# Kernel optimization log

Hardware: AMD Instinct MI355X
Metric: run time of the kernel (lower is better)

## Reference

```python
import jax, jax.numpy as jnp
import numpy as np

B, S, DM, DC = 16, 4096, 1280, 768
N_AOE, N_IMG, N_DELTA = 16, 16, 16
ANAT_GATE, DIS_GATE, DELTA_SCALE = 0.5, 0.5, 1.0


def setup_inputs() -> dict:
    key = jax.random.key(0)
    ks = jax.random.split(key, 9)
    def lin(k, fan_in, fan_out):
        return jax.random.normal(k, (fan_in, fan_out), jnp.float32) / np.sqrt(fan_in)
    return {
        "hidden_states": jax.random.normal(ks[0], (B, S, DM), jnp.float32),
        "encoder_hidden_states": jax.random.normal(ks[1], (B, N_AOE + N_IMG + N_DELTA, DC), jnp.float32),
        "w_q": lin(ks[2], DM, DM),
        "w_k": lin(ks[3], DC, DM),
        "w_v": lin(ks[4], DC, DM),
        "w_k_dis": lin(ks[5], DC, DM),
        "w_v_dis": lin(ks[6], DC, DM),
        "w_out": lin(ks[7], DM, DM),
        "b_out": jnp.zeros((DM,), jnp.float32),
        "n_heads": 8,
    }


def _heads(x, h):
    b, s, d = x.shape
    return x.reshape(b, s, h, d // h).transpose(0, 2, 1, 3)  # [B,H,S,dh]


def _attend(q, k, v, scale):
    # q:[B,H,Sq,dh], k/v:[B,H,Sk,dh], Sk small (16)
    scores = jnp.einsum("bhqd,bhkd->bhqk", q, k) * scale
    probs = jax.nn.softmax(scores, axis=-1)
    return jnp.einsum("bhqk,bhkd->bhqd", probs, v)


def reference(hidden_states, encoder_hidden_states, w_q, w_k, w_v,
              w_k_dis, w_v_dis, w_out, b_out, n_heads):
    residual = hidden_states
    dh = DM // n_heads
    scale = 1.0 / np.sqrt(dh)

    dis_tok = encoder_hidden_states[:, :N_AOE, :]
    anat_tok = encoder_hidden_states[:, N_AOE:N_AOE + N_IMG, :]
    delta_tok = encoder_hidden_states[:, -N_DELTA:, :]

    q = _heads(hidden_states @ w_q, n_heads)
    z_anat = _attend(q, _heads(anat_tok @ w_k, n_heads), _heads(anat_tok @ w_v, n_heads), scale)
    z_dis = _attend(q, _heads(dis_tok @ w_k_dis, n_heads), _heads(dis_tok @ w_v_dis, n_heads), scale)
    z_delta = _attend(q, _heads(delta_tok @ w_k_dis, n_heads), _heads(delta_tok @ w_v_dis, n_heads), scale)

    z = ANAT_GATE * z_anat + DIS_GATE * z_dis + DELTA_SCALE * z_delta
    out = z.transpose(0, 2, 1, 3).reshape(hidden_states.shape[0], -1, DM)
    out = out @ w_out + b_out  # to_out[0]; to_out[1] dropout = identity in eval
    return out + residual  # residual_connection, rescale_output_factor=1.0
```

## Files before the change

kernel.cpp:

```cpp
#include <hip/hip_runtime.h>
#include <hip/hip_bf16.h>

#define B_ 16
#define S_ 4096
#define DM_ 1280
#define DC_ 768
#define NC_ 384
#define SCALE_ 0.07905694150420949f

typedef __attribute__((ext_vector_type(8))) short bf16x8;
typedef __attribute__((ext_vector_type(4))) float f32x4;
typedef __attribute__((ext_vector_type(4))) unsigned short u16x4;

#define S_BARRIER() asm volatile("s_barrier" ::: "memory")
#define WAIT_VM(n) asm volatile("s_waitcnt vmcnt(" #n ")" ::: "memory")
#define WAIT_LGKM0() asm volatile("s_waitcnt lgkmcnt(0)" ::: "memory")

__device__ __forceinline__ unsigned short f2bf(float f) {
    unsigned int u = __builtin_bit_cast(unsigned int, f);
    u = (u + 0x7FFFu + ((u >> 16) & 1u)) >> 16;
    return (unsigned short)u;
}

__device__ __forceinline__ bf16x8 pack8(float4 x0, float4 x1) {
    bf16x8 a;
    a[0] = __builtin_bit_cast(short, __float2bfloat16(x0.x));
    a[1] = __builtin_bit_cast(short, __float2bfloat16(x0.y));
    a[2] = __builtin_bit_cast(short, __float2bfloat16(x0.z));
    a[3] = __builtin_bit_cast(short, __float2bfloat16(x0.w));
    a[4] = __builtin_bit_cast(short, __float2bfloat16(x1.x));
    a[5] = __builtin_bit_cast(short, __float2bfloat16(x1.y));
    a[6] = __builtin_bit_cast(short, __float2bfloat16(x1.z));
    a[7] = __builtin_bit_cast(short, __float2bfloat16(x1.w));
    return a;
}

__device__ __forceinline__ void gload16(const void* g, void* l) {
    __builtin_amdgcn_global_load_lds(
        (const __attribute__((address_space(1))) void*)g,
        (__attribute__((address_space(3))) void*)l, 16, 0, 0);
}

__device__ __forceinline__ void tcvt_body(const float* __restrict__ in,
                                          unsigned short* __restrict__ out,
                                          int R, int C, int bx, int by, int tid) {
    __shared__ float tile[32][33];
    int c0 = bx * 32, r0 = by * 32;
    int tx = tid & 31, ty = tid >> 5;
    for (int i = ty; i < 32; i += 8)
        tile[i][tx] = in[(size_t)(r0 + i) * C + c0 + tx];
    __syncthreads();
    for (int i = ty; i < 32; i += 8)
        out[(size_t)(c0 + i) * R + r0 + tx] = f2bf(tile[tx][i]);
}

__global__ __launch_bounds__(256)
void k_prep(const float* __restrict__ wq, const float* __restrict__ wk,
            const float* __restrict__ wv, const float* __restrict__ wkd,
            const float* __restrict__ wvd, const float* __restrict__ wout,
            unsigned short* __restrict__ wq_bf, unsigned short* __restrict__ wTk,
            unsigned short* __restrict__ wTv, unsigned short* __restrict__ wTkd,
            unsigned short* __restrict__ wTvd, unsigned short* __restrict__ woutT) {
    int bid = blockIdx.x, tid = threadIdx.x;
    if (bid < 1600) {
        int i = bid * 256 + tid;
        float4 v = ((const float4*)wq)[i];
        u16x4 o = { f2bf(v.x), f2bf(v.y), f2bf(v.z), f2bf(v.w) };
        ((u16x4*)wq_bf)[i] = o;
    } else if (bid < 2560) {
        int r = bid - 1600; tcvt_body(wk,  wTk,  DC_, DM_, r % 40, r / 40, tid);
    } else if (bid < 3520) {
        int r = bid - 2560; tcvt_body(wv,  wTv,  DC_, DM_, r % 40, r / 40, tid);
    } else if (bid < 4480) {
        int r = bid - 3520; tcvt_body(wkd, wTkd, DC_, DM_, r % 40, r / 40, tid);
    } else if (bid < 5440) {
        int r = bid - 4480; tcvt_body(wvd, wTvd, DC_, DM_, r % 40, r / 40, tid);
    } else {
        int r = bid - 5440; tcvt_body(wout, woutT, DM_, DM_, r % 40, r / 40, tid);
    }
}

__global__ __launch_bounds__(256)
void k_projM(const float* __restrict__ enc,
             const unsigned short* __restrict__ wTk, const unsigned short* __restrict__ wTv,
             const unsigned short* __restrict__ wTkd, const unsigned short* __restrict__ wTvd,
             unsigned short* __restrict__ KV) {
    int bid = blockIdx.x;
    int j = bid / 80, rem = bid % 80, b = rem / 5, nt = rem % 5;
    int tid = threadIdx.x, w = tid >> 6, l = tid & 63, l15 = l & 15, l4 = l >> 4;
    int tok0 = (j < 2) ? 16 : ((j < 4) ? 0 : 32);
    const unsigned short* wT = (j == 0) ? wTk : (j == 1) ? wTv : (j == 2 || j == 4) ? wTkd : wTvd;
    const float* ap = enc + ((size_t)(b * 48 + tok0 + l15)) * DC_;
    f32x4 zero = {0.f, 0.f, 0.f, 0.f};
    f32x4 acc[4];
    #pragma unroll
    for (int t = 0; t < 4; t++) acc[t] = zero;
    for (int kk = 0; kk < 24; kk++) {
        const float4* hp = (const float4*)(ap + kk * 32 + l4 * 8);
        bf16x8 af = pack8(hp[0], hp[1]);
        #pragma unroll
        for (int t = 0; t < 4; t++) {
            int n0 = nt * 256 + w * 64 + t * 16;
            bf16x8 bf = *(const bf16x8*)(wT + (size_t)(n0 + l15) * DC_ + kk * 32 + l4 * 8);
            acc[t] = __builtin_amdgcn_mfma_f32_16x16x32_bf16(af, bf, acc[t], 0, 0, 0);
        }
    }
    #pragma unroll
    for (int t = 0; t < 4; t++) {
        int e = nt * 256 + w * 64 + t * 16 + l15;
        #pragma unroll
        for (int r = 0; r < 4; r++)
            KV[((size_t)(j * 16 + b) * 16 + l4 * 4 + r) * DM_ + e] = f2bf(acc[t][r]);
    }
}

__global__ __launch_bounds__(256)
void k_au(const unsigned short* __restrict__ KV, const unsigned short* __restrict__ wqbf,
          const unsigned short* __restrict__ woutT,
          unsigned short* __restrict__ At2, unsigned short* __restrict__ Ut2) {
    int bid0 = blockIdx.x;
    bool isA = bid0 < 384;
    int bid = isA ? bid0 : bid0 - 384;
    int b = bid & 15, r_ = bid >> 4, x = r_ >> 3, h = r_ & 7;
    int tid = threadIdx.x, w = tid >> 6, l = tid & 63, l15 = l & 15, l4 = l >> 4;
    int xh = x * 8 + h;
    int jrow = isA ? (2 * x) : (2 * x + 1);
    const unsigned short* wmat = isA ? wqbf : woutT;
    float postscale = isA ? SCALE_ : ((x == 2) ? 1.0f : 0.5f);
    bf16x8 bfr[5];
    #pragma unroll
    for (int kk = 0; kk < 5; kk++)
        bfr[kk] = *(const bf16x8*)(KV + ((size_t)(jrow * 16 + b) * 16 + l15) * DM_ + h * 160 + kk * 32 + l4 * 8);
    f32x4 zero = {0.f, 0.f, 0.f, 0.f};
    for (int tt = 0; tt < 20; tt++) {
        int d0 = w * 320 + tt * 16;
        f32x4 acc = zero;
        if (isA) {
            #pragma unroll
            for (int kk = 0; kk < 5; kk++) {
                bf16x8 af = *(const bf16x8*)(wmat + (size_t)(d0 + l15) * DM_ + h * 160 + kk * 32 + l4 * 8);
                acc = __builtin_amdgcn_mfma_f32_16x16x32_bf16(af, bfr[kk], acc, 0, 0, 0);
            }
            int c = xh * 16 + l15;
            u16x4 pk;
            #pragma unroll
            for (int r = 0; r < 4; r++) pk[r] = f2bf(acc[r] * postscale);
            *(u16x4*)(At2 + ((size_t)(b * 40 + (d0 >> 5)) * NC_ + c) * 32 + (d0 & 31) + l4 * 4) = pk;
        } else {
            #pragma unroll
            for (int kk = 0; kk < 5; kk++) {
                bf16x8 af = *(const bf16x8*)(wmat + (size_t)(d0 + l15) * DM_ + h * 160 + kk * 32 + l4 * 8);
                acc = __builtin_amdgcn_mfma_f32_16x16x32_bf16(bfr[kk], af, acc, 0, 0, 0);
            }
            int e = d0 + l15;
            u16x4 pk;
            #pragma unroll
            for (int r = 0; r < 4; r++) pk[r] = f2bf(acc[r] * postscale);
            *(u16x4*)(Ut2 + ((size_t)(b * 12 + (xh >> 1)) * DM_ + e) * 32 + (xh & 1) * 16 + l4 * 4) = pk;
        }
    }
}

__global__ __launch_bounds__(256, 2)
void k_scores7(const float* __restrict__ hid, const unsigned short* __restrict__ At2,
               unsigned short* __restrict__ P2) {
    __shared__ char smem[73728];
    unsigned short* Apnl = (unsigned short*)smem;
    char* Hlds = smem + 49152;
    int bid = blockIdx.x;
    int orig = (bid & 7) * 128 + (bid >> 3);
    int b = orig >> 6, st = orig & 63;
    int s0 = st * 64;
    int tid = threadIdx.x, w = tid >> 6, l = tid & 63, l15 = l & 15, l4 = l >> 4;
    int rdsw = (l4 ^ ((l15 >> 1) & 3)) * 8;
    const unsigned short* Ab = At2 + (size_t)b * 40 * NC_ * 32;
    const float* hsrc = hid + ((size_t)b * S_ + s0) * DM_;
    f32x4 zero = {0.f, 0.f, 0.f, 0.f};
    f32x4 acc[4][6];
    #pragma unroll
    for (int si = 0; si < 4; si++)
        #pragma unroll
        for (int cj = 0; cj < 6; cj++) acc[si][cj] = zero;

    auto stageA = [&](int kk, int ab) {
        const unsigned short* slab = Ab + (size_t)kk * (NC_ * 32);
        #pragma unroll
        for (int i = 0; i < 6; i++) {
            int idx = i * 256 + tid;
            int c = idx >> 2, m = (idx & 3) ^ ((c >> 1) & 3);
            gload16(slab + (size_t)c * 32 + m * 8, smem + ab * 24576 + idx * 16);
        }
    };
    auto stageH = [&](int kk, int hb) {
        #pragma unroll
        for (int i = 0; i < 2; i++) {
            int idx = i * 256 + tid;
            int r = idx >> 3, sg = (idx & 7) ^ (r & 7);
            gload16(hsrc + (size_t)r * DM_ + kk * 32 + sg * 4, Hlds + hb * 8192 + idx * 16);
        }
    };
    auto compute = [&](int ab, int hb) {
        bf16x8 hpk[4];
        #pragma unroll
        for (int si = 0; si < 4; si++) {
            int r = si * 16 + l15;
            float4 lo = *(const float4*)(Hlds + hb * 8192 + r * 128 + (((2 * l4) ^ (l15 & 7)) * 16));
            float4 hi = *(const float4*)(Hlds + hb * 8192 + r * 128 + (((2 * l4 + 1) ^ (l15 & 7)) * 16));
            hpk[si] = pack8(lo, hi);
        }
        __builtin_amdgcn_s_setprio(1);
        #pragma unroll
        for (int cj = 0; cj < 6; cj++) {
            bf16x8 af = *(const bf16x8*)&Apnl[ab * 12288 + (w * 96 + cj * 16 + l15) * 32 + rdsw];
            #pragma unroll
            for (int si = 0; si < 4; si++)
                acc[si][cj] = __builtin_amdgcn_mfma_f32_16x16x32_bf16(af, hpk[si], acc[si][cj], 0, 0, 0);
        }
        __builtin_amdgcn_s_setprio(0);
    };
    auto SITER = [&](int kk) {
        stageA(kk + 1, (kk + 1) & 1);
        stageH(kk + 2, (kk + 2) % 3);
        WAIT_VM(10);
        S_BARRIER();
        compute(kk & 1, kk % 3);
        WAIT_LGKM0();
        S_BARRIER();
    };

    stageA(0, 0); stageH(0, 0); stageH(1, 1);
    for (int k0 = 0; k0 < 36; k0 += 6) {
        SITER(k0 + 0); SITER(k0 + 1); SITER(k0 + 2);
        SITER(k0 + 3); SITER(k0 + 4); SITER(k0 + 5);
    }
    SITER(36); SITER(37);
    stageA(39, 1);
    WAIT_VM(8);
    S_BARRIER();
    compute(0, 38 % 3);
    WAIT_LGKM0();
    S_BARRIER();
    WAIT_VM(0);
    S_BARRIER();
    compute(1, 39 % 3);
    WAIT_LGKM0();
    S_BARRIER();

    #pragma unroll
    for (int si = 0; si < 4; si++) {
        int s_l = si * 16 + l15;
        #pragma unroll
        for (int cj = 0; cj < 6; cj++) {
            float v0 = acc[si][cj][0], v1 = acc[si][cj][1], v2 = acc[si][cj][2], v3 = acc[si][cj][3];
            float mx = fmaxf(fmaxf(v0, v1), fmaxf(v2, v3));
            mx = fmaxf(mx, __shfl_xor(mx, 16));
            mx = fmaxf(mx, __shfl_xor(mx, 32));
            float e0 = __expf(v0 - mx), e1 = __expf(v1 - mx), e2 = __expf(v2 - mx), e3 = __expf(v3 - mx);
            float sm = e0 + e1 + e2 + e3;
            sm += __shfl_xor(sm, 16);
            sm += __shfl_xor(sm, 32);
            float rs = 1.0f / sm;
            u16x4 pk = { f2bf(e0 * rs), f2bf(e1 * rs), f2bf(e2 * rs), f2bf(e3 * rs) };
            int c = w * 96 + cj * 16 + l4 * 4;
            int chunk = ((c & 31) >> 3) ^ (s_l & 3);
            *(u16x4*)(smem + (c >> 5) * 4096 + s_l * 64 + chunk * 16 + (l4 & 1) * 8) = pk;
        }
    }
    __syncthreads();

    unsigned short* P2b = P2 + (size_t)b * 12 * S_ * 32;
    #pragma unroll
    for (int i = 0; i < 12; i++) {
        int sl = tid >> 2, m = tid & 3;
        uint4 v = *(const uint4*)(smem + i * 4096 + sl * 64 + ((m ^ (sl & 3)) * 16));
        *(uint4*)(P2b + ((size_t)i * S_ + s0 + sl) * 32 + m * 8) = v;
    }
}

__global__ __launch_bounds__(256, 3)
void k_pv4(const unsigned short* __restrict__ P2, const unsigned short* __restrict__ Ut2,
           const float* __restrict__ hid, const float* __restrict__ bo,
           float* __restrict__ out) {
    __shared__ unsigned short Plds[3 * 4096];
    __shared__ unsigned short Ulds[3 * 4096];
    int bid = blockIdx.x;
    int orig = (bid & 7) * 640 + (bid >> 3);
    int b = orig / 320, rem = orig % 320;
    int st = rem / 10, ec = rem % 10;
    int s0 = st * 128, e0 = ec * 128;
    int tid = threadIdx.x, w = tid >> 6, l = tid & 63, l15 = l & 15, l4 = l >> 4;
    int wr = w >> 1, wc = w & 1;
    int rdsw = (l4 ^ ((l15 >> 1) & 3)) * 8;
    const unsigned short* Pb = P2 + (size_t)b * 12 * S_ * 32;
    const unsigned short* Ub = Ut2 + (size_t)b * 12 * DM_ * 32;
    f32x4 zero = {0.f, 0.f, 0.f, 0.f};
    f32x4 acc[4][4];
    #pragma unroll
    for (int si = 0; si < 4; si++)
        #pragma unroll
        for (int ej = 0; ej < 4; ej++) acc[si][ej] = zero;

    auto stage = [&](int kk, int bufsel) {
        const unsigned short* Pslab = Pb + (size_t)kk * S_ * 32;
        const unsigned short* Uslab = Ub + (size_t)kk * DM_ * 32;
        #pragma unroll
        for (int i = 0; i < 2; i++) {
            int idx = i * 256 + tid;
            int r = idx >> 2, m = (idx & 3) ^ ((r >> 1) & 3);
            gload16(Pslab + ((size_t)s0 + r) * 32 + m * 8, (char*)Plds + bufsel * 8192 + idx * 16);
            gload16(Uslab + ((size_t)e0 + r) * 32 + m * 8, (char*)Ulds + bufsel * 8192 + idx * 16);
        }
    };
    auto compute = [&](int cur) {
        bf16x8 uf[4], pf[4];
        #pragma unroll
        for (int ej = 0; ej < 4; ej++)
            uf[ej] = *(const bf16x8*)&Ulds[cur * 4096 + (wr * 64 + ej * 16 + l15) * 32 + rdsw];
        #pragma unroll
        for (int si = 0; si < 4; si++)
            pf[si] = *(const bf16x8*)&Plds[cur * 4096 + (wc * 64 + si * 16 + l15) * 32 + rdsw];
        __builtin_amdgcn_s_setprio(1);
        #pragma unroll
        for (int si = 0; si < 4; si++)
            #pragma unroll
            for (int ej = 0; ej < 4; ej++)
                acc[si][ej] = __builtin_amdgcn_mfma_f32_16x16x32_bf16(uf[ej], pf[si], acc[si][ej], 0, 0, 0);
        __builtin_amdgcn_s_setprio(0);
    };
    auto PITER = [&](int kk, int cur, int tgt) {
        stage(kk + 2, tgt);
        WAIT_VM(8);
        S_BARRIER();
        compute(cur);
        WAIT_LGKM0();
        S_BARRIER();
    };

    stage(0, 0); stage(1, 1);
    for (int k0 = 0; k0 < 9; k0 += 3) {
        PITER(k0 + 0, 0, 2); PITER(k0 + 1, 1, 0); PITER(k0 + 2, 2, 1);
    }
    PITER(9, 0, 2);
    WAIT_VM(4); S_BARRIER(); compute(1); WAIT_LGKM0(); S_BARRIER();
    WAIT_VM(0); S_BARRIER(); compute(2);

    float4 b4[4];
    #pragma unroll
    for (int ej = 0; ej < 4; ej++)
        b4[ej] = *(const float4*)(bo + e0 + wr * 64 + ej * 16 + l4 * 4);
    #pragma unroll
    for (int si = 0; si < 4; si++) {
        int srow = s0 + wc * 64 + si * 16 + l15;
        #pragma unroll
        for (int ej = 0; ej < 4; ej++) {
            int ecol = e0 + wr * 64 + ej * 16 + l4 * 4;
            size_t off = ((size_t)b * S_ + srow) * DM_ + ecol;
            float4 h4 = *(const float4*)(hid + off);
            f32x4 a = acc[si][ej];
            float4 o4;
            o4.x = a[0] + b4[ej].x + h4.x;
            o4.y = a[1] + b4[ej].y + h4.y;
            o4.z = a[2] + b4[ej].z + h4.z;
            o4.w = a[3] + b4[ej].w + h4.w;
            *(float4*)(out + off) = o4;
        }
    }
}

extern "C" void kernel_launch(void* const* d_in, const int* in_sizes, int n_in,
                              void* d_out, int out_size, void* d_ws, size_t ws_size,
                              hipStream_t stream) {
    const float* hid  = (const float*)d_in[0];
    const float* enc  = (const float*)d_in[1];
    const float* wq   = (const float*)d_in[2];
    const float* wk   = (const float*)d_in[3];
    const float* wv   = (const float*)d_in[4];
    const float* wkd  = (const float*)d_in[5];
    const float* wvd  = (const float*)d_in[6];
    const float* wout = (const float*)d_in[7];
    const float* bo   = (const float*)d_in[8];
    float* out = (float*)d_out;

    char* ws = (char*)d_ws;
    unsigned short* At2    = (unsigned short*)(ws);
    unsigned short* Ut2    = (unsigned short*)(ws + 15728640);
    unsigned short* KV     = (unsigned short*)(ws + 31457280);
    unsigned short* wq_bf  = (unsigned short*)(ws + 35389440);
    unsigned short* woutT  = (unsigned short*)(ws + 38666240);
    unsigned short* wTk    = (unsigned short*)(ws + 41943040);
    unsigned short* wTv    = (unsigned short*)(ws + 43909120);
    unsigned short* wTkd   = (unsigned short*)(ws + 45875200);
    unsigned short* wTvd   = (unsigned short*)(ws + 47841280);
    unsigned short* P2     = (unsigned short*)(ws + 35389440);

    k_prep<<<7040, 256, 0, stream>>>(wq, wk, wv, wkd, wvd, wout,
                                     wq_bf, wTk, wTv, wTkd, wTvd, woutT);
    k_projM<<<480, 256, 0, stream>>>(enc, wTk, wTv, wTkd, wTvd, KV);
    k_au<<<768, 256, 0, stream>>>(KV, wq_bf, woutT, At2, Ut2);
    k_scores7<<<1024, 256, 0, stream>>>(hid, At2, P2);
    k_pv4<<<5120, 256, 0, stream>>>(P2, Ut2, hid, bo, out);
}
```

Before: 399.6 us.

## Double sequence tile in scores kernel to reuse A panel across 128 rows

The scores kernel now processes 128 sequence rows per block instead of 64, so each staged A panel slab feeds twice as many MFMAs and global A traffic is halved. The hidden-state pipeline drops from triple to double buffering, and the softmax output is written directly to global memory instead of being staged through LDS. The costs are doubled accumulator registers (48 f32x4) at two blocks per CU, half as many blocks, a shallower prefetch depth, and narrower 8-byte global stores for P.

```diff
diff --git a/kernel.cpp b/kernel.cpp
--- a/kernel.cpp
+++ b/kernel.cpp
@@ -162,25 +162,25 @@
 }
 
 __global__ __launch_bounds__(256, 2)
-void k_scores7(const float* __restrict__ hid, const unsigned short* __restrict__ At2,
+void k_scores8(const float* __restrict__ hid, const unsigned short* __restrict__ At2,
                unsigned short* __restrict__ P2) {
-    __shared__ char smem[73728];
+    __shared__ char smem[81920];
     unsigned short* Apnl = (unsigned short*)smem;
     char* Hlds = smem + 49152;
     int bid = blockIdx.x;
-    int orig = (bid & 7) * 128 + (bid >> 3);
-    int b = orig >> 6, st = orig & 63;
-    int s0 = st * 64;
+    int orig = (bid & 7) * 64 + (bid >> 3);
+    int b = orig >> 5, st = orig & 31;
+    int s0 = st * 128;
     int tid = threadIdx.x, w = tid >> 6, l = tid & 63, l15 = l & 15, l4 = l >> 4;
     int rdsw = (l4 ^ ((l15 >> 1) & 3)) * 8;
     const unsigned short* Ab = At2 + (size_t)b * 40 * NC_ * 32;
     const float* hsrc = hid + ((size_t)b * S_ + s0) * DM_;
     f32x4 zero = {0.f, 0.f, 0.f, 0.f};
-    f32x4 acc[4][6];
-    #pragma unroll
-    for (int si = 0; si < 4; si++)
-        #pragma unroll
-        for (int cj = 0; cj < 6; cj++) acc[si][cj] = zero;
+    f32x4 acc[8][6];
+    #pragma unroll
+    for (int g = 0; g < 8; g++)
+        #pragma unroll
+        for (int cj = 0; cj < 6; cj++) acc[g][cj] = zero;
 
     auto stageA = [&](int kk, int ab) {
         const unsigned short* slab = Ab + (size_t)kk * (NC_ * 32);
@@ -193,65 +193,58 @@
     };
     auto stageH = [&](int kk, int hb) {
         #pragma unroll
-        for (int i = 0; i < 2; i++) {
+        for (int i = 0; i < 4; i++) {
             int idx = i * 256 + tid;
             int r = idx >> 3, sg = (idx & 7) ^ (r & 7);
-            gload16(hsrc + (size_t)r * DM_ + kk * 32 + sg * 4, Hlds + hb * 8192 + idx * 16);
+            gload16(hsrc + (size_t)r * DM_ + kk * 32 + sg * 4, Hlds + hb * 16384 + idx * 16);
         }
     };
     auto compute = [&](int ab, int hb) {
-        bf16x8 hpk[4];
-        #pragma unroll
-        for (int si = 0; si < 4; si++) {
-            int r = si * 16 + l15;
-            float4 lo = *(const float4*)(Hlds + hb * 8192 + r * 128 + (((2 * l4) ^ (l15 & 7)) * 16));
-            float4 hi = *(const float4*)(Hlds + hb * 8192 + r * 128 + (((2 * l4 + 1) ^ (l15 & 7)) * 16));
-            hpk[si] = pack8(lo, hi);
-        }
-        __builtin_amdgcn_s_setprio(1);
-        #pragma unroll
-        for (int cj = 0; cj < 6; cj++) {
-            bf16x8 af = *(const bf16x8*)&Apnl[ab * 12288 + (w * 96 + cj * 16 + l15) * 32 + rdsw];
-            #pragma unroll
-            for (int si = 0; si < 4; si++)
-                acc[si][cj] = __builtin_amdgcn_mfma_f32_16x16x32_bf16(af, hpk[si], acc[si][cj], 0, 0, 0);
-        }
-        __builtin_amdgcn_s_setprio(0);
+        #pragma unroll
+        for (int sh = 0; sh < 2; sh++) {
+            bf16x8 hpk[4];
+            #pragma unroll
+            for (int si = 0; si < 4; si++) {
+                int r = sh * 64 + si * 16 + l15;
+                float4 lo = *(const float4*)(Hlds + hb * 16384 + r * 128 + (((2 * l4) ^ (l15 & 7)) * 16));
+                float4 hi = *(const float4*)(Hlds + hb * 16384 + r * 128 + (((2 * l4 + 1) ^ (l15 & 7)) * 16));
+                hpk[si] = pack8(lo, hi);
+            }
+            __builtin_amdgcn_s_setprio(1);
+            #pragma unroll
+            for (int cj = 0; cj < 6; cj++) {
+                bf16x8 af = *(const bf16x8*)&Apnl[ab * 12288 + (w * 96 + cj * 16 + l15) * 32 + rdsw];
+                #pragma unroll
+                for (int si = 0; si < 4; si++)
+                    acc[sh * 4 + si][cj] = __builtin_amdgcn_mfma_f32_16x16x32_bf16(af, hpk[si], acc[sh * 4 + si][cj], 0, 0, 0);
+            }
+            __builtin_amdgcn_s_setprio(0);
+        }
     };
     auto SITER = [&](int kk) {
         stageA(kk + 1, (kk + 1) & 1);
-        stageH(kk + 2, (kk + 2) % 3);
+        stageH(kk + 1, (kk + 1) & 1);
         WAIT_VM(10);
         S_BARRIER();
-        compute(kk & 1, kk % 3);
+        compute(kk & 1, kk & 1);
         WAIT_LGKM0();
         S_BARRIER();
     };
 
-    stageA(0, 0); stageH(0, 0); stageH(1, 1);
-    for (int k0 = 0; k0 < 36; k0 += 6) {
-        SITER(k0 + 0); SITER(k0 + 1); SITER(k0 + 2);
-        SITER(k0 + 3); SITER(k0 + 4); SITER(k0 + 5);
-    }
-    SITER(36); SITER(37);
-    stageA(39, 1);
-    WAIT_VM(8);
-    S_BARRIER();
-    compute(0, 38 % 3);
-    WAIT_LGKM0();
-    S_BARRIER();
+    stageA(0, 0); stageH(0, 0);
+    for (int k0 = 0; k0 < 38; k0 += 2) { SITER(k0); SITER(k0 + 1); }
+    SITER(38);
     WAIT_VM(0);
     S_BARRIER();
-    compute(1, 39 % 3);
-    WAIT_LGKM0();
-    S_BARRIER();
-
-    #pragma unroll
-    for (int si = 0; si < 4; si++) {
-        int s_l = si * 16 + l15;
+    compute(1, 1);
+
+    unsigned short* P2b = P2 + (size_t)b * 12 * S_ * 32;
+    #pragma unroll
+    for (int g = 0; g < 8; g++) {
+        int s_l = (g >> 2) * 64 + (g & 3) * 16 + l15;
         #pragma unroll
         for (int cj = 0; cj < 6; cj++) {
-            float v0 = acc[si][cj][0], v1 = acc[si][cj][1], v2 = acc[si][cj][2], v3 = acc[si][cj][3];
+            float v0 = acc[g][cj][0], v1 = acc[g][cj][1], v2 = acc[g][cj][2], v3 = acc[g][cj][3];
             float mx = fmaxf(fmaxf(v0, v1), fmaxf(v2, v3));
             mx = fmaxf(mx, __shfl_xor(mx, 16));
             mx = fmaxf(mx, __shfl_xor(mx, 32));
@@ -261,19 +254,10 @@
             sm += __shfl_xor(sm, 32);
             float rs = 1.0f / sm;
             u16x4 pk = { f2bf(e0 * rs), f2bf(e1 * rs), f2bf(e2 * rs), f2bf(e3 * rs) };
-            int c = w * 96 + cj * 16 + l4 * 4;
-            int chunk = ((c & 31) >> 3) ^ (s_l & 3);
-            *(u16x4*)(smem + (c >> 5) * 4096 + s_l * 64 + chunk * 16 + (l4 & 1) * 8) = pk;
-        }
-    }
-    __syncthreads();
-
-    unsigned short* P2b = P2 + (size_t)b * 12 * S_ * 32;
-    #pragma unroll
-    for (int i = 0; i < 12; i++) {
-        int sl = tid >> 2, m = tid & 3;
-        uint4 v = *(const uint4*)(smem + i * 4096 + sl * 64 + ((m ^ (sl & 3)) * 16));
-        *(uint4*)(P2b + ((size_t)i * S_ + s0 + sl) * 32 + m * 8) = v;
+            int kk2 = w * 3 + (cj >> 1);
+            int c32 = (cj & 1) * 16 + l4 * 4;
+            *(u16x4*)(P2b + ((size_t)kk2 * S_ + s0 + s_l) * 32 + c32) = pk;
+        }
     }
 }
 
@@ -397,6 +381,6 @@
                                      wq_bf, wTk, wTv, wTkd, wTvd, woutT);
     k_projM<<<480, 256, 0, stream>>>(enc, wTk, wTv, wTkd, wTvd, KV);
     k_au<<<768, 256, 0, stream>>>(KV, wq_bf, woutT, At2, Ut2);
-    k_scores7<<<1024, 256, 0, stream>>>(hid, At2, P2);
+    k_scores8<<<512, 256, 0, stream>>>(hid, At2, P2);
     k_pv4<<<5120, 256, 0, stream>>>(P2, Ut2, hid, bo, out);
 }
```

Measured after the change: 555.9 us. 39.1% more time.
